# Optimization experiments

Measured on AMD Instinct MI355X. Metric: run time of the kernel, lower is better.

The kernel has to match this reference:

```python
import jax, jax.numpy as jnp
import numpy as np

NUM_HEADS = 12
NUM_LANDMARKS = 64
DIM = 768


def _iterative_inv(mat, n_iter=6):
    # mat: [B, H, L, L]
    L = mat.shape[-1]
    I = jnp.eye(L, dtype=mat.dtype)
    K = mat
    # init: V = K^T / max_j(sum_i K_ij), scalar per (B, H)
    denom = jnp.max(jnp.sum(K, axis=-2), axis=-1)[:, :, None, None]
    V = (1.0 / denom) * jnp.swapaxes(K, -1, -2)
    for _ in range(n_iter):
        KV = jnp.matmul(K, V)
        V = jnp.matmul(0.25 * V, 13.0 * I - jnp.matmul(KV, 15.0 * I - jnp.matmul(KV, 7.0 * I - KV)))
    return V


def setup_inputs() -> dict:
    key = jax.random.key(0)
    k1, k2, k3, k4 = jax.random.split(key, 4)
    B, N, C = 4, 4096, DIM
    x = jax.random.normal(k1, (B, N, C), dtype=jnp.float32)
    w_qkv = jax.random.normal(k2, (3 * C, C), dtype=jnp.float32) * (C ** -0.5)
    w_proj = jax.random.normal(k3, (C, C), dtype=jnp.float32) * (C ** -0.5)
    b_proj = jax.random.normal(k4, (C,), dtype=jnp.float32) * 0.01
    return {"x": x, "w_qkv": w_qkv, "w_proj": w_proj, "b_proj": b_proj}


def reference(x, w_qkv, w_proj, b_proj):
    B, N, C = x.shape
    H, Lm = NUM_HEADS, NUM_LANDMARKS
    hd = C // H
    scale = hd ** 0.5
    # qkv: [3, B, H, N, hd]
    qkv = (x @ w_qkv.T).reshape(B, N, 3, H, hd).transpose(2, 0, 3, 1, 4)
    q, k, v = qkv[0], qkv[1], qkv[2]
    q = q / scale  # scaling happens BEFORE landmark pooling, as in source
    segs = N // Lm  # N % Lm == 0 path
    keys_landmarks = k.reshape(B, H, Lm, segs, hd).mean(axis=-2)      # [B,H,Lm,hd]
    queries_landmarks = q.reshape(B, H, Lm, segs, hd).mean(axis=-2)   # [B,H,Lm,hd]
    kernel_1 = jax.nn.softmax(jnp.einsum('bhnd,bhld->bhnl', q, keys_landmarks), axis=-1)            # [B,H,N,Lm]
    kernel_2 = jax.nn.softmax(jnp.einsum('bhmd,bhld->bhml', queries_landmarks, keys_landmarks), axis=-1)  # [B,H,Lm,Lm]
    kernel_3 = jax.nn.softmax(jnp.einsum('bhld,bhnd->bhln', queries_landmarks, k), axis=-1)         # [B,H,Lm,N]
    out = jnp.matmul(jnp.matmul(kernel_1, _iterative_inv(kernel_2)), jnp.matmul(kernel_3, v))       # [B,H,N,hd]
    out = out.transpose(0, 2, 1, 3).reshape(B, N, C)
    return out @ w_proj.T + b_proj
```

## Files before the change

### kernel.cpp

```cpp
#include <hip/hip_runtime.h>
#include <hip/hip_bf16.h>

#define DI __device__ __forceinline__

typedef __attribute__((ext_vector_type(8))) short bh8;
typedef __attribute__((ext_vector_type(8))) unsigned short us8;
typedef __attribute__((ext_vector_type(4))) float f4ev;

static constexpr int Bn = 4;
static constexpr int Nn = 4096;
static constexpr int Cn = 768;
static constexpr int Hn = 12;
static constexpr int Dn = 64;
static constexpr int Ln = 64;
static constexpr int TOKS = Bn * Nn;
static constexpr int BHn = Bn * Hn;

static constexpr size_t SZ_XB  = (size_t)TOKS * Cn * 2;
static constexpr size_t SZ_QKV = (size_t)BHn * Nn * Dn * 2;
static constexpr size_t OFF_XB   = 0;
static constexpr size_t OFF_QB   = OFF_XB + SZ_XB;
static constexpr size_t OFF_KB   = OFF_QB + SZ_QKV;
static constexpr size_t OFF_VB   = OFF_KB + SZ_QKV;
static constexpr size_t OFF_WQB  = OFF_VB + SZ_QKV;
static constexpr size_t OFF_WPB  = OFF_WQB + (size_t)3 * Cn * Cn * 2;
static constexpr size_t OFF_XM   = OFF_WPB + (size_t)Cn * Cn * 2;
static constexpr size_t OFF_QL   = OFF_XM + (size_t)Bn * Ln * Cn * 4;
static constexpr size_t OFF_KL   = OFF_QL + (size_t)Bn * Ln * Cn * 4;
static constexpr size_t OFF_VINV = OFF_KL + (size_t)Bn * Ln * Cn * 4;
static constexpr size_t OFF_CP   = OFF_VINV + (size_t)BHn * 64 * 64 * 4;
static constexpr size_t OFF_W2   = OFF_CP + (size_t)BHn * 32 * 64 * 2 * 4;

DI unsigned short f2bf(float f) {
  __hip_bfloat16 h = __float2bfloat16(f);
  return *reinterpret_cast<unsigned short*>(&h);
}
DI float bf2f(unsigned short u) {
  union { unsigned int i; float f; } c; c.i = ((unsigned)u) << 16; return c.f;
}

DI void gload_lds16(const void* g, void* l) {
  __builtin_amdgcn_global_load_lds((const __attribute__((address_space(1))) void*)g,
                                   (__attribute__((address_space(3))) void*)l, 16, 0, 0);
}

__global__ void cast_k(const float* __restrict__ s, unsigned short* __restrict__ d, int n4) {
  int i = blockIdx.x * blockDim.x + threadIdx.x;
  int st = gridDim.x * blockDim.x;
  const float4* s4 = (const float4*)s;
  ushort4* d4 = (ushort4*)d;
  for (; i < n4; i += st) {
    float4 v = s4[i];
    ushort4 o; o.x = f2bf(v.x); o.y = f2bf(v.y); o.z = f2bf(v.z); o.w = f2bf(v.w);
    d4[i] = o;
  }
}

__global__ void castmean_k(const float* __restrict__ x, unsigned short* __restrict__ xb,
                           float* __restrict__ xm) {
  int bl = blockIdx.x, cz = blockIdx.y;
  int c = cz * 384 + threadIdx.x * 2;
  const float* xp = x + (size_t)bl * 64 * Cn + c;
  unsigned short* xbp = xb + (size_t)bl * 64 * Cn + c;
  float s0 = 0.f, s1 = 0.f;
  #pragma unroll 8
  for (int r = 0; r < 64; ++r) {
    float2 v = *(const float2*)(xp + (size_t)r * Cn);
    ushort2 o; o.x = f2bf(v.x); o.y = f2bf(v.y);
    *(ushort2*)(xbp + (size_t)r * Cn) = o;
    s0 += v.x; s1 += v.y;
  }
  xm[(size_t)bl * Cn + c]     = s0 * 0.015625f;
  xm[(size_t)bl * Cn + c + 1] = s1 * 0.015625f;
}

__launch_bounds__(256)
__global__ void landgemm_k(const float* __restrict__ xm, const float* __restrict__ wqkv,
                           float* __restrict__ part) {
  __shared__ float XT[64][65];
  __shared__ float WT[64][65];
  int b = blockIdx.x, ct = blockIdx.y, kc = blockIdx.z;
  int t = threadIdx.x;
  int tr = t >> 4, tc = t & 15;
  int r0 = tr * 4, j0 = tc * 4;
  const float* xb_ = xm + (size_t)b * Ln * Cn + kc * 64;
  const float* wb_ = wqkv + (size_t)ct * 64 * Cn + kc * 64;
  #pragma unroll
  for (int i = t; i < 1024; i += 256) {
    int r = i >> 4, c4 = (i & 15) * 4;
    float4 xv = *(const float4*)(xb_ + (size_t)r * Cn + c4);
    XT[c4 + 0][r] = xv.x; XT[c4 + 1][r] = xv.y; XT[c4 + 2][r] = xv.z; XT[c4 + 3][r] = xv.w;
    float4 wv = *(const float4*)(wb_ + (size_t)r * Cn + c4);
    WT[c4 + 0][r] = wv.x; WT[c4 + 1][r] = wv.y; WT[c4 + 2][r] = wv.z; WT[c4 + 3][r] = wv.w;
  }
  __syncthreads();
  float acc[4][4];
  #pragma unroll
  for (int i = 0; i < 4; ++i)
    #pragma unroll
    for (int j = 0; j < 4; ++j) acc[i][j] = 0.f;
  for (int cc = 0; cc < 64; ++cc) {
    float4 a4 = *(const float4*)&XT[cc][r0];
    float4 b4 = *(const float4*)&WT[cc][j0];
    acc[0][0] += a4.x * b4.x; acc[0][1] += a4.x * b4.y; acc[0][2] += a4.x * b4.z; acc[0][3] += a4.x * b4.w;
    acc[1][0] += a4.y * b4.x; acc[1][1] += a4.y * b4.y; acc[1][2] += a4.y * b4.z; acc[1][3] += a4.y * b4.w;
    acc[2][0] += a4.z * b4.x; acc[2][1] += a4.z * b4.y; acc[2][2] += a4.z * b4.z; acc[2][3] += a4.z * b4.w;
    acc[3][0] += a4.w * b4.x; acc[3][1] += a4.w * b4.y; acc[3][2] += a4.w * b4.z; acc[3][3] += a4.w * b4.w;
  }
  float* op = part + ((size_t)kc * 256 + b * Ln) * 1536 + (size_t)ct * 64;
  #pragma unroll
  for (int i = 0; i < 4; ++i)
    *(float4*)(op + (size_t)(r0 + i) * 1536 + j0) = make_float4(acc[i][0], acc[i][1], acc[i][2], acc[i][3]);
}

__global__ void landred_k(const float* __restrict__ part, float* __restrict__ ql,
                          float* __restrict__ kl) {
  int i4 = blockIdx.x * 256 + threadIdx.x;
  const float4* p4 = (const float4*)part;
  float4 s = p4[i4];
  #pragma unroll
  for (int kc = 1; kc < 12; ++kc) {
    float4 v = p4[(size_t)kc * 98304 + i4];
    s.x += v.x; s.y += v.y; s.z += v.z; s.w += v.w;
  }
  int row = i4 / 384, c = (i4 % 384) * 4;
  if (c < 768) {
    s.x *= 0.125f; s.y *= 0.125f; s.z *= 0.125f; s.w *= 0.125f;
    *(float4*)(ql + (size_t)row * Cn + c) = s;
  } else {
    *(float4*)(kl + (size_t)row * Cn + (c - 768)) = s;
  }
}

__launch_bounds__(256)
__global__ void k2inv_k(const float* __restrict__ ql, const float* __restrict__ kl,
                        float* __restrict__ vinv) {
  __shared__ float B0[64][68], B1[64][68], B2[64][68], B3[64][68],
                   B4[64][68], B5[64][68], B6[64][68], B7[64][68];
  __shared__ float dinv_s;
  float (*Qt)[68] = B0, (*Kt)[68] = B1;
  float (*KV)[68] = B0, (*KVt)[68] = B1;
  float (*K2)[68] = B2, (*K2t)[68] = B3;
  float (*Vv)[68] = B4, (*Vt)[68] = B5;
  float (*T1)[68] = B6, (*Uu)[68] = B7;

  int bh = blockIdx.x, b = bh / Hn, h = bh % Hn;
  int t = threadIdx.x;
  int tr = t >> 4, tc = t & 15;
  int r0 = tr * 4, j0 = tc * 4;

  {
    const float* qbase = ql + (size_t)(b * Ln) * Cn + h * Dn;
    const float* kbase = kl + (size_t)(b * Ln) * Cn + h * Dn;
    #pragma unroll
    for (int it = 0; it < 4; ++it) {
      int idx = it * 256 + t;
      int l = idx >> 4, d0 = (idx & 15) * 4;
      float4 qv = *(const float4*)(qbase + (size_t)l * Cn + d0);
      float4 kv = *(const float4*)(kbase + (size_t)l * Cn + d0);
      Qt[d0 + 0][l] = qv.x; Qt[d0 + 1][l] = qv.y; Qt[d0 + 2][l] = qv.z; Qt[d0 + 3][l] = qv.w;
      Kt[d0 + 0][l] = kv.x; Kt[d0 + 1][l] = kv.y; Kt[d0 + 2][l] = kv.z; Kt[d0 + 3][l] = kv.w;
    }
  }
  __syncthreads();

  float acc[4][4];
  #define MM64(LT, RR)                                                     \
    {                                                                      \
      _Pragma("unroll")                                                    \
      for (int i_ = 0; i_ < 4; ++i_)                                       \
        _Pragma("unroll")                                                  \
        for (int j_ = 0; j_ < 4; ++j_) acc[i_][j_] = 0.f;                  \
      for (int c_ = 0; c_ < 64; c_ += 4) {                                 \
        _Pragma("unroll")                                                  \
        for (int cc_ = 0; cc_ < 4; ++cc_) {                                \
          float4 a4 = *(const float4*)&LT[c_ + cc_][r0];                   \
          float4 b4 = *(const float4*)&RR[c_ + cc_][j0];                   \
          acc[0][0] += a4.x * b4.x; acc[0][1] += a4.x * b4.y;              \
          acc[0][2] += a4.x * b4.z; acc[0][3] += a4.x * b4.w;              \
          acc[1][0] += a4.y * b4.x; acc[1][1] += a4.y * b4.y;              \
          acc[1][2] += a4.y * b4.z; acc[1][3] += a4.y * b4.w;              \
          acc[2][0] += a4.z * b4.x; acc[2][1] += a4.z * b4.y;              \
          acc[2][2] += a4.z * b4.z; acc[2][3] += a4.z * b4.w;              \
          acc[3][0] += a4.w * b4.x; acc[3][1] += a4.w * b4.y;              \
          acc[3][2] += a4.w * b4.z; acc[3][3] += a4.w * b4.w;              \
        }                                                                  \
      }                                                                    \
    }

  MM64(Qt, Kt);
  #pragma unroll
  for (int i = 0; i < 4; ++i)
    *(float4*)&K2[r0 + i][j0] = make_float4(acc[i][0], acc[i][1], acc[i][2], acc[i][3]);
  __syncthreads();

  if (t < 64) {
    float m = -1e30f;
    #pragma unroll
    for (int c4 = 0; c4 < 16; ++c4) {
      float4 v = *(const float4*)&K2[t][c4 * 4];
      m = fmaxf(m, fmaxf(fmaxf(v.x, v.y), fmaxf(v.z, v.w)));
    }
    float s = 0.f;
    #pragma unroll
    for (int c4 = 0; c4 < 16; ++c4) {
      float4 v = *(const float4*)&K2[t][c4 * 4];
      v.x = __expf(v.x - m); v.y = __expf(v.y - m);
      v.z = __expf(v.z - m); v.w = __expf(v.w - m);
      s += v.x + v.y + v.z + v.w;
      *(float4*)&K2[t][c4 * 4] = v;
    }
    float inv = 1.f / s;
    #pragma unroll
    for (int c4 = 0; c4 < 16; ++c4) {
      float4 v = *(const float4*)&K2[t][c4 * 4];
      v.x *= inv; v.y *= inv; v.z *= inv; v.w *= inv;
      *(float4*)&K2[t][c4 * 4] = v;
      K2t[c4 * 4 + 0][t] = v.x; K2t[c4 * 4 + 1][t] = v.y;
      K2t[c4 * 4 + 2][t] = v.z; K2t[c4 * 4 + 3][t] = v.w;
    }
  }
  __syncthreads();
  if (t < 64) {
    float cs = 0.f;
    #pragma unroll
    for (int c4 = 0; c4 < 16; ++c4) {
      float4 v = *(const float4*)&K2t[t][c4 * 4];
      cs += v.x + v.y + v.z + v.w;
    }
    #pragma unroll
    for (int off = 1; off < 64; off <<= 1) cs = fmaxf(cs, __shfl_xor(cs, off));
    if (t == 0) dinv_s = 1.f / cs;
  }
  __syncthreads();
  float dinv = dinv_s;
  #pragma unroll
  for (int jj = 0; jj < 4; ++jj) {
    float4 k4 = *(const float4*)&K2[j0 + jj][r0];
    k4.x *= dinv; k4.y *= dinv; k4.z *= dinv; k4.w *= dinv;
    *(float4*)&Vt[j0 + jj][r0] = k4;
    Vv[r0 + 0][j0 + jj] = k4.x; Vv[r0 + 1][j0 + jj] = k4.y;
    Vv[r0 + 2][j0 + jj] = k4.z; Vv[r0 + 3][j0 + jj] = k4.w;
  }
  __syncthreads();

  float nv[4][4];
  for (int itn = 0; itn < 6; ++itn) {
    MM64(K2t, Vv);
    #pragma unroll
    for (int i = 0; i < 4; ++i)
      *(float4*)&KV[r0 + i][j0] = make_float4(acc[i][0], acc[i][1], acc[i][2], acc[i][3]);
    #pragma unroll
    for (int jj = 0; jj < 4; ++jj)
      *(float4*)&KVt[j0 + jj][r0] = make_float4(acc[0][jj], acc[1][jj], acc[2][jj], acc[3][jj]);
    __syncthreads();
    MM64(KVt, KV);
    #pragma unroll
    for (int i = 0; i < 4; ++i) {
      float4 kv4 = *(const float4*)&KV[r0 + i][j0];
      *(float4*)&T1[r0 + i][j0] = make_float4(7.f * kv4.x - acc[i][0], 7.f * kv4.y - acc[i][1],
                                              7.f * kv4.z - acc[i][2], 7.f * kv4.w - acc[i][3]);
    }
    __syncthreads();
    MM64(KVt, T1);
    #pragma unroll
    for (int i = 0; i < 4; ++i) {
      float4 kv4 = *(const float4*)&KV[r0 + i][j0];
      *(float4*)&Uu[r0 + i][j0] = make_float4(15.f * kv4.x - acc[i][0], 15.f * kv4.y - acc[i][1],
                                              15.f * kv4.z - acc[i][2], 15.f * kv4.w - acc[i][3]);
    }
    __syncthreads();
    MM64(Vt, Uu);
    #pragma unroll
    for (int i = 0; i < 4; ++i) {
      float4 v4 = *(const float4*)&Vv[r0 + i][j0];
      nv[i][0] = 0.25f * (13.f * v4.x - acc[i][0]);
      nv[i][1] = 0.25f * (13.f * v4.y - acc[i][1]);
      nv[i][2] = 0.25f * (13.f * v4.z - acc[i][2]);
      nv[i][3] = 0.25f * (13.f * v4.w - acc[i][3]);
    }
    __syncthreads();
    #pragma unroll
    for (int i = 0; i < 4; ++i)
      *(float4*)&Vv[r0 + i][j0] = make_float4(nv[i][0], nv[i][1], nv[i][2], nv[i][3]);
    #pragma unroll
    for (int jj = 0; jj < 4; ++jj)
      *(float4*)&Vt[j0 + jj][r0] = make_float4(nv[0][jj], nv[1][jj], nv[2][jj], nv[3][jj]);
    __syncthreads();
  }
  float* op = vinv + (size_t)bh * 4096;
  #pragma unroll
  for (int i = 0; i < 4; ++i)
    *(float4*)(op + (size_t)(r0 + i) * 64 + j0) = make_float4(nv[i][0], nv[i][1], nv[i][2], nv[i][3]);
  #undef MM64
}

__launch_bounds__(256)
__global__ void gemm_qkv_k(const __hip_bfloat16* __restrict__ A, const __hip_bfloat16* __restrict__ W,
                           __hip_bfloat16* __restrict__ qb, __hip_bfloat16* __restrict__ kb,
                           __hip_bfloat16* __restrict__ vb) {
  __shared__ unsigned short As[2][128][64], Bs[2][128][64];
  int t = threadIdx.x, lane = t & 63, w = t >> 6;
  int wr = w >> 1, wc = w & 1;
  int m0 = blockIdx.x * 128, n0 = blockIdx.y * 128;
  int srow = w * 8 + (lane >> 3);
  int scol = ((lane & 7) ^ ((lane >> 3) & 7)) * 8;
  f4ev acc[4][4];
  f4ev zz = {0.f, 0.f, 0.f, 0.f};
  #pragma unroll
  for (int m = 0; m < 4; ++m)
    #pragma unroll
    for (int n = 0; n < 4; ++n) acc[m][n] = zz;
  const __hip_bfloat16* ga = A + (size_t)(m0 + srow) * Cn + scol;
  const __hip_bfloat16* gb = W + (size_t)(n0 + srow) * Cn + scol;

  #pragma unroll
  for (int c = 0; c < 4; ++c) {
    gload_lds16(ga + (size_t)(c * 32) * Cn, &As[0][c * 32 + w * 8][0]);
    gload_lds16(gb + (size_t)(c * 32) * Cn, &Bs[0][c * 32 + w * 8][0]);
  }
  __syncthreads();
  int cur = 0;
  for (int it = 0; it < 12; ++it) {
    if (it < 11) {
      int k0 = (it + 1) * 64;
      #pragma unroll
      for (int c = 0; c < 4; ++c) {
        gload_lds16(ga + (size_t)(c * 32) * Cn + k0, &As[cur ^ 1][c * 32 + w * 8][0]);
        gload_lds16(gb + (size_t)(c * 32) * Cn + k0, &Bs[cur ^ 1][c * 32 + w * 8][0]);
      }
    }
    #pragma unroll
    for (int ks = 0; ks < 2; ++ks) {
      int pc = ((ks * 4 + (lane >> 4)) ^ (lane & 7)) * 8;
      bh8 af[4], bf_[4];
      #pragma unroll
      for (int m = 0; m < 4; ++m)
        af[m] = *(const bh8*)&As[cur][wr * 64 + m * 16 + (lane & 15)][pc];
      #pragma unroll
      for (int n = 0; n < 4; ++n)
        bf_[n] = *(const bh8*)&Bs[cur][wc * 64 + n * 16 + (lane & 15)][pc];
      #pragma unroll
      for (int m = 0; m < 4; ++m)
        #pragma unroll
        for (int n = 0; n < 4; ++n)
          acc[m][n] = __builtin_amdgcn_mfma_f32_16x16x32_bf16(af[m], bf_[n], acc[m][n], 0, 0, 0);
    }
    __syncthreads();
    cur ^= 1;
  }
  int which = (n0 >= 1536) ? 2 : (n0 >= 768 ? 1 : 0);
  __hip_bfloat16* dst = which == 0 ? qb : (which == 1 ? kb : vb);
  float sc = which == 0 ? 0.125f : 1.f;
  #pragma unroll
  for (int m = 0; m < 4; ++m) {
    int rbase = m0 + wr * 64 + m * 16 + ((lane >> 4) << 2);
    #pragma unroll
    for (int n = 0; n < 4; ++n) {
      int c = n0 + wc * 64 + n * 16 + (lane & 15);
      int rem = c - which * 768;
      int h = rem >> 6, dd = rem & 63;
      #pragma unroll
      for (int jj = 0; jj < 4; ++jj) {
        int r = rbase + jj;
        int b = r >> 12, ntok = r & 4095;
        dst[(((size_t)(b * Hn + h) * Nn + ntok) << 6) + dd] = __float2bfloat16(acc[m][n][jj] * sc);
      }
    }
  }
}

__launch_bounds__(256)
__global__ void k3vflash_k(const float* __restrict__ ql, const __hip_bfloat16* __restrict__ kb,
                           const __hip_bfloat16* __restrict__ vb,
                           float* __restrict__ ocp, float* __restrict__ stat) {
  __shared__ unsigned short Ks[128][72];
  __shared__ unsigned short VT[64][136];
  auto Pl = (unsigned short (*)[136]) & Ks[0][0];
  int ch = blockIdx.x, bh = blockIdx.y;
  int b = bh / Hn, h = bh % Hn;
  int t = threadIdx.x, lane = t & 63, w = t >> 6;

  {
    int row = t >> 1, half = (t & 1) * 32;
    const us8* krow = (const us8*)((const unsigned short*)kb + ((size_t)bh * Nn + (size_t)ch * 128 + row) * Dn + half);
    const us8* vrow = (const us8*)((const unsigned short*)vb + ((size_t)bh * Nn + (size_t)ch * 128 + row) * Dn + half);
    us8 kv0 = krow[0], kv1 = krow[1], kv2 = krow[2], kv3 = krow[3];
    us8 vv0 = vrow[0], vv1 = vrow[1], vv2 = vrow[2], vv3 = vrow[3];
    *(us8*)&Ks[row][half + 0]  = kv0;
    *(us8*)&Ks[row][half + 8]  = kv1;
    *(us8*)&Ks[row][half + 16] = kv2;
    *(us8*)&Ks[row][half + 24] = kv3;
    #pragma unroll
    for (int e = 0; e < 8; ++e) {
      VT[half + e][row]      = vv0[e];
      VT[half + 8 + e][row]  = vv1[e];
      VT[half + 16 + e][row] = vv2[e];
      VT[half + 24 + e][row] = vv3[e];
    }
  }
  bh8 aq[2];
  {
    const float* qrow = ql + ((size_t)(b * Ln + w * 16 + (lane & 15))) * Cn + h * Dn + (lane >> 4) * 8;
    #pragma unroll
    for (int ks = 0; ks < 2; ++ks) {
      float4 f0 = *(const float4*)(qrow + ks * 32);
      float4 f1 = *(const float4*)(qrow + ks * 32 + 4);
      bh8 v;
      v[0] = (short)f2bf(f0.x); v[1] = (short)f2bf(f0.y); v[2] = (short)f2bf(f0.z); v[3] = (short)f2bf(f0.w);
      v[4] = (short)f2bf(f1.x); v[5] = (short)f2bf(f1.y); v[6] = (short)f2bf(f1.z); v[7] = (short)f2bf(f1.w);
      aq[ks] = v;
    }
  }
  __syncthreads();
  f4ev sacc[8];
  f4ev zz = {0.f, 0.f, 0.f, 0.f};
  #pragma unroll
  for (int nt = 0; nt < 8; ++nt) sacc[nt] = zz;
  #pragma unroll
  for (int ks = 0; ks < 2; ++ks)
    #pragma unroll
    for (int nt = 0; nt < 8; ++nt) {
      bh8 bk = *(const bh8*)&Ks[nt * 16 + (lane & 15)][ks * 32 + (lane >> 4) * 8];
      sacc[nt] = __builtin_amdgcn_mfma_f32_16x16x32_bf16(aq[ks], bk, sacc[nt], 0, 0, 0);
    }
  float M[4];
  #pragma unroll
  for (int j = 0; j < 4; ++j) {
    float m = sacc[0][j];
    #pragma unroll
    for (int nt = 1; nt < 8; ++nt) m = fmaxf(m, sacc[nt][j]);
    m = fmaxf(m, __shfl_xor(m, 1));
    m = fmaxf(m, __shfl_xor(m, 2));
    m = fmaxf(m, __shfl_xor(m, 4));
    m = fmaxf(m, __shfl_xor(m, 8));
    M[j] = m;
  }
  __syncthreads();
  float Ssum[4] = {0.f, 0.f, 0.f, 0.f};
  #pragma unroll
  for (int nt = 0; nt < 8; ++nt)
    #pragma unroll
    for (int j = 0; j < 4; ++j) {
      float pf = __expf(sacc[nt][j] - M[j]);
      Ssum[j] += pf;
      Pl[w * 16 + (lane >> 4) * 4 + j][nt * 16 + (lane & 15)] = f2bf(pf);
    }
  #pragma unroll
  for (int j = 0; j < 4; ++j) {
    float s = Ssum[j];
    s += __shfl_xor(s, 1);
    s += __shfl_xor(s, 2);
    s += __shfl_xor(s, 4);
    s += __shfl_xor(s, 8);
    Ssum[j] = s;
  }
  if ((lane & 15) == 0) {
    #pragma unroll
    for (int j = 0; j < 4; ++j) {
      int l2 = w * 16 + (lane >> 4) * 4 + j;
      float* sp = stat + (((size_t)bh * 32 + ch) * 64 + l2) * 2;
      sp[0] = M[j]; sp[1] = Ssum[j];
    }
  }
  __syncthreads();
  f4ev oacc[4];
  #pragma unroll
  for (int nt = 0; nt < 4; ++nt) oacc[nt] = zz;
  #pragma unroll
  for (int ks = 0; ks < 4; ++ks) {
    bh8 ap = *(const bh8*)&Pl[w * 16 + (lane & 15)][ks * 32 + (lane >> 4) * 8];
    #pragma unroll
    for (int nt = 0; nt < 4; ++nt) {
      bh8 bv = *(const bh8*)&VT[nt * 16 + (lane & 15)][ks * 32 + (lane >> 4) * 8];
      oacc[nt] = __builtin_amdgcn_mfma_f32_16x16x32_bf16(ap, bv, oacc[nt], 0, 0, 0);
    }
  }
  float* ob = ocp + (((size_t)bh * 32 + ch) * 64) * 64;
  #pragma unroll
  for (int nt = 0; nt < 4; ++nt)
    #pragma unroll
    for (int j = 0; j < 4; ++j) {
      int l2 = w * 16 + ((lane >> 4) << 2) + j;
      ob[l2 * 64 + nt * 16 + (lane & 15)] = oacc[nt][j];
    }
}

__global__ void w2f_k(const float* __restrict__ ocp, const float* __restrict__ stat,
                      const float* __restrict__ vinv, float* __restrict__ w2) {
  __shared__ float kv[64][72], vi[64][72];
  __shared__ float wch[32][64];
  __shared__ float invS[64];
  int bh = blockIdx.x, t = threadIdx.x, j = t & 63, ig = t >> 6;
  if (t < 64) {
    const float* sp = stat + (size_t)bh * 32 * 128;
    float M = -1e30f;
    #pragma unroll
    for (int c = 0; c < 32; ++c) M = fmaxf(M, sp[c * 128 + t * 2]);
    float S = 0.f;
    #pragma unroll
    for (int c = 0; c < 32; ++c) {
      float wcb = __expf(sp[c * 128 + t * 2] - M);
      wch[c][t] = wcb;
      S += wcb * sp[c * 128 + t * 2 + 1];
    }
    invS[t] = 1.f / S;
  }
  for (int i = t; i < 4096; i += 256) vi[i >> 6][i & 63] = vinv[(size_t)bh * 4096 + i];
  __syncthreads();
  float acc[16];
  #pragma unroll
  for (int i = 0; i < 16; ++i) acc[i] = 0.f;
  const float* op = ocp + (size_t)bh * 32 * 4096;
  for (int c = 0; c < 32; ++c) {
    #pragma unroll
    for (int jj = 0; jj < 4; ++jj) {
      int i4 = t * 4 + jj * 1024;
      float4 v = *(const float4*)(op + (size_t)c * 4096 + i4);
      float wcb = wch[c][i4 >> 6];
      acc[jj * 4 + 0] += v.x * wcb;
      acc[jj * 4 + 1] += v.y * wcb;
      acc[jj * 4 + 2] += v.z * wcb;
      acc[jj * 4 + 3] += v.w * wcb;
    }
  }
  #pragma unroll
  for (int jj = 0; jj < 4; ++jj) {
    int i4 = t * 4 + jj * 1024;
    float is = invS[i4 >> 6];
    kv[i4 >> 6][(i4 & 63) + 0] = acc[jj * 4 + 0] * is;
    kv[i4 >> 6][(i4 & 63) + 1] = acc[jj * 4 + 1] * is;
    kv[i4 >> 6][(i4 & 63) + 2] = acc[jj * 4 + 2] * is;
    kv[i4 >> 6][(i4 & 63) + 3] = acc[jj * 4 + 3] * is;
  }
  __syncthreads();
  float a[16];
  #pragma unroll
  for (int li = 0; li < 16; ++li) a[li] = 0.f;
  for (int c2 = 0; c2 < 64; ++c2) {
    float vv = kv[c2][j];
    #pragma unroll
    for (int li = 0; li < 16; ++li) a[li] += vi[ig * 16 + li][c2] * vv;
  }
  #pragma unroll
  for (int li = 0; li < 16; ++li) w2[(size_t)bh * 4096 + (ig * 16 + li) * 64 + j] = a[li];
}

__launch_bounds__(256)
__global__ void k1app_k(const __hip_bfloat16* __restrict__ qb, const float* __restrict__ kl,
                        const float* __restrict__ w2, __hip_bfloat16* __restrict__ oh) {
  __shared__ unsigned short SM[128 * 72 + 64 * 72 * 2];
  auto Klhi = (unsigned short (*)[72])(SM);
  auto Kllo = (unsigned short (*)[72])(SM + 64 * 72);
  auto Pl   = (unsigned short (*)[72])(SM);
  auto Whi  = (unsigned short (*)[72])(SM + 128 * 72);
  auto Wlo  = (unsigned short (*)[72])(SM + 128 * 72 + 64 * 72);

  int ch = blockIdx.x, bh = blockIdx.y;
  int b = bh / Hn, h = bh % Hn;
  int t = threadIdx.x, lane = t & 63, w = t >> 6;

  {
    const float* klb = kl + (size_t)(b * Ln) * Cn + h * Dn;
    const float* w2b = w2 + (size_t)bh * 4096;
    #pragma unroll
    for (int it = 0; it < 4; ++it) {
      int idx = it * 256 + t;
      int l = idx >> 4, d0 = (idx & 15) * 4;
      float4 kv = *(const float4*)(klb + (size_t)l * Cn + d0);
      ushort4 hi4; ushort4 lo4;
      hi4.x = f2bf(kv.x); lo4.x = f2bf(kv.x - bf2f(hi4.x));
      hi4.y = f2bf(kv.y); lo4.y = f2bf(kv.y - bf2f(hi4.y));
      hi4.z = f2bf(kv.z); lo4.z = f2bf(kv.z - bf2f(hi4.z));
      hi4.w = f2bf(kv.w); lo4.w = f2bf(kv.w - bf2f(hi4.w));
      *(ushort4*)&Klhi[l][d0] = hi4;
      *(ushort4*)&Kllo[l][d0] = lo4;
      float4 wv = *(const float4*)(w2b + (size_t)l * 64 + d0);
      unsigned short h0 = f2bf(wv.x), h1 = f2bf(wv.y), h2 = f2bf(wv.z), h3 = f2bf(wv.w);
      Whi[d0 + 0][l] = h0; Wlo[d0 + 0][l] = f2bf(wv.x - bf2f(h0));
      Whi[d0 + 1][l] = h1; Wlo[d0 + 1][l] = f2bf(wv.y - bf2f(h1));
      Whi[d0 + 2][l] = h2; Wlo[d0 + 2][l] = f2bf(wv.z - bf2f(h2));
      Whi[d0 + 3][l] = h3; Wlo[d0 + 3][l] = f2bf(wv.w - bf2f(h3));
    }
  }
  bh8 aq[2][2];
  {
    const unsigned short* qbase = (const unsigned short*)qb + ((size_t)bh * Nn + (size_t)ch * 128) * Dn;
    #pragma unroll
    for (int m = 0; m < 2; ++m)
      #pragma unroll
      for (int ks = 0; ks < 2; ++ks)
        aq[m][ks] = *(const bh8*)(qbase + (size_t)(w * 32 + m * 16 + (lane & 15)) * Dn + ks * 32 + (lane >> 4) * 8);
  }
  __syncthreads();
  f4ev sacc[2][4];
  f4ev zz = {0.f, 0.f, 0.f, 0.f};
  #pragma unroll
  for (int m = 0; m < 2; ++m)
    #pragma unroll
    for (int nt = 0; nt < 4; ++nt) sacc[m][nt] = zz;
  #pragma unroll
  for (int ks = 0; ks < 2; ++ks)
    #pragma unroll
    for (int nt = 0; nt < 4; ++nt) {
      bh8 bhi = *(const bh8*)&Klhi[nt * 16 + (lane & 15)][ks * 32 + (lane >> 4) * 8];
      bh8 blo = *(const bh8*)&Kllo[nt * 16 + (lane & 15)][ks * 32 + (lane >> 4) * 8];
      #pragma unroll
      for (int m = 0; m < 2; ++m) {
        sacc[m][nt] = __builtin_amdgcn_mfma_f32_16x16x32_bf16(aq[m][ks], bhi, sacc[m][nt], 0, 0, 0);
        sacc[m][nt] = __builtin_amdgcn_mfma_f32_16x16x32_bf16(aq[m][ks], blo, sacc[m][nt], 0, 0, 0);
      }
    }
  float Pn[2][4][4];
  #pragma unroll
  for (int m = 0; m < 2; ++m)
    #pragma unroll
    for (int j = 0; j < 4; ++j) {
      float mx = sacc[m][0][j];
      #pragma unroll
      for (int nt = 1; nt < 4; ++nt) mx = fmaxf(mx, sacc[m][nt][j]);
      mx = fmaxf(mx, __shfl_xor(mx, 1));
      mx = fmaxf(mx, __shfl_xor(mx, 2));
      mx = fmaxf(mx, __shfl_xor(mx, 4));
      mx = fmaxf(mx, __shfl_xor(mx, 8));
      float sum = 0.f;
      #pragma unroll
      for (int nt = 0; nt < 4; ++nt) {
        float e = __expf(sacc[m][nt][j] - mx);
        Pn[m][nt][j] = e;
        sum += e;
      }
      sum += __shfl_xor(sum, 1);
      sum += __shfl_xor(sum, 2);
      sum += __shfl_xor(sum, 4);
      sum += __shfl_xor(sum, 8);
      float inv = 1.f / sum;
      #pragma unroll
      for (int nt = 0; nt < 4; ++nt) Pn[m][nt][j] *= inv;
    }
  __syncthreads();
  #pragma unroll
  for (int m = 0; m < 2; ++m)
    #pragma unroll
    for (int nt = 0; nt < 4; ++nt)
      #pragma unroll
      for (int j = 0; j < 4; ++j)
        Pl[w * 32 + m * 16 + (lane >> 4) * 4 + j][nt * 16 + (lane & 15)] = f2bf(Pn[m][nt][j]);
  __syncthreads();
  f4ev oacc[2][4];
  #pragma unroll
  for (int m = 0; m < 2; ++m)
    #pragma unroll
    for (int nt = 0; nt < 4; ++nt) oacc[m][nt] = zz;
  #pragma unroll
  for (int ks = 0; ks < 2; ++ks) {
    bh8 ap[2];
    #pragma unroll
    for (int m = 0; m < 2; ++m)
      ap[m] = *(const bh8*)&Pl[w * 32 + m * 16 + (lane & 15)][ks * 32 + (lane >> 4) * 8];
    #pragma unroll
    for (int nt = 0; nt < 4; ++nt) {
      bh8 bhi = *(const bh8*)&Whi[nt * 16 + (lane & 15)][ks * 32 + (lane >> 4) * 8];
      bh8 blo = *(const bh8*)&Wlo[nt * 16 + (lane & 15)][ks * 32 + (lane >> 4) * 8];
      #pragma unroll
      for (int m = 0; m < 2; ++m) {
        oacc[m][nt] = __builtin_amdgcn_mfma_f32_16x16x32_bf16(ap[m], bhi, oacc[m][nt], 0, 0, 0);
        oacc[m][nt] = __builtin_amdgcn_mfma_f32_16x16x32_bf16(ap[m], blo, oacc[m][nt], 0, 0, 0);
      }
    }
  }
  unsigned short* ohb = (unsigned short*)oh;
  #pragma unroll
  for (int m = 0; m < 2; ++m)
    #pragma unroll
    for (int nt = 0; nt < 4; ++nt)
      #pragma unroll
      for (int j = 0; j < 4; ++j) {
        int tok = ch * 128 + w * 32 + m * 16 + (lane >> 4) * 4 + j;
        int dd = nt * 16 + (lane & 15);
        ohb[((size_t)(b * Nn + tok)) * Cn + h * Dn + dd] = f2bf(oacc[m][nt][j]);
      }
}

__launch_bounds__(256)
__global__ void gemm_proj_k(const __hip_bfloat16* __restrict__ A, const __hip_bfloat16* __restrict__ W,
                            const float* __restrict__ bias, float* __restrict__ out) {
  __shared__ unsigned short As[128][32], Bs[128][32];
  int orig = blockIdx.x;
  int wg = (orig & 7) * 96 + (orig >> 3);
  int mt = wg / 6, ntile = wg % 6;
  int m0 = mt * 128, n0 = ntile * 128;
  int t = threadIdx.x, lane = t & 63, w = t >> 6;
  int wr = w >> 1, wc = w & 1;
  int srow = lane >> 2;
  int scol = (((lane & 3) ^ ((lane >> 3) & 3))) * 8;
  int rcol = (((lane >> 4) ^ ((lane >> 1) & 3))) * 8;
  f4ev acc[4][4];
  f4ev zz = {0.f, 0.f, 0.f, 0.f};
  #pragma unroll
  for (int m = 0; m < 4; ++m)
    #pragma unroll
    for (int n = 0; n < 4; ++n) acc[m][n] = zz;
  const __hip_bfloat16* ga = A + (size_t)(m0 + w * 16 + srow) * Cn + scol;
  const __hip_bfloat16* gb = W + (size_t)(n0 + w * 16 + srow) * Cn + scol;
  for (int k0 = 0; k0 < Cn; k0 += 32) {
    gload_lds16(ga + k0,                   &As[w * 16][0]);
    gload_lds16(ga + (size_t)64 * Cn + k0, &As[64 + w * 16][0]);
    gload_lds16(gb + k0,                   &Bs[w * 16][0]);
    gload_lds16(gb + (size_t)64 * Cn + k0, &Bs[64 + w * 16][0]);
    __syncthreads();
    bh8 af[4], bf_[4];
    #pragma unroll
    for (int m = 0; m < 4; ++m)
      af[m] = *(const bh8*)&As[wr * 64 + m * 16 + (lane & 15)][rcol];
    #pragma unroll
    for (int n = 0; n < 4; ++n)
      bf_[n] = *(const bh8*)&Bs[wc * 64 + n * 16 + (lane & 15)][rcol];
    #pragma unroll
    for (int m = 0; m < 4; ++m)
      #pragma unroll
      for (int n = 0; n < 4; ++n)
        acc[m][n] = __builtin_amdgcn_mfma_f32_16x16x32_bf16(af[m], bf_[n], acc[m][n], 0, 0, 0);
    __syncthreads();
  }
  #pragma unroll
  for (int m = 0; m < 4; ++m) {
    int rbase = m0 + wr * 64 + m * 16 + ((lane >> 4) << 2);
    #pragma unroll
    for (int n = 0; n < 4; ++n) {
      int c = n0 + wc * 64 + n * 16 + (lane & 15);
      float bv = bias[c];
      #pragma unroll
      for (int jj = 0; jj < 4; ++jj)
        out[(size_t)(rbase + jj) * Cn + c] = acc[m][n][jj] + bv;
    }
  }
}

extern "C" void kernel_launch(void* const* d_in, const int* in_sizes, int n_in,
                              void* d_out, int out_size, void* d_ws, size_t ws_size,
                              hipStream_t stream) {
  const float* x     = (const float*)d_in[0];
  const float* wqkv  = (const float*)d_in[1];
  const float* wproj = (const float*)d_in[2];
  const float* bproj = (const float*)d_in[3];
  float* out = (float*)d_out;
  char* ws = (char*)d_ws;

  auto xb   = (__hip_bfloat16*)(ws + OFF_XB);
  auto qb   = (__hip_bfloat16*)(ws + OFF_QB);
  auto kb   = (__hip_bfloat16*)(ws + OFF_KB);
  auto vb   = (__hip_bfloat16*)(ws + OFF_VB);
  auto wqb  = (__hip_bfloat16*)(ws + OFF_WQB);
  auto wpb  = (__hip_bfloat16*)(ws + OFF_WPB);
  auto ocp  = (float*)(ws + OFF_XB);
  auto oh   = (__hip_bfloat16*)(ws + OFF_XB);
  auto part = (float*)(ws + OFF_QB);
  auto xm   = (float*)(ws + OFF_XM);
  auto ql   = (float*)(ws + OFF_QL);
  auto kl   = (float*)(ws + OFF_KL);
  auto vinv = (float*)(ws + OFF_VINV);
  auto cp   = (float*)(ws + OFF_CP);
  auto w2   = (float*)(ws + OFF_W2);

  castmean_k<<<dim3(256, 2), 192, 0, stream>>>(x, (unsigned short*)xb, xm);
  cast_k<<<1024, 256, 0, stream>>>(wqkv, (unsigned short*)wqb, 3 * Cn * Cn / 4);
  cast_k<<<512, 256, 0, stream>>>(wproj, (unsigned short*)wpb, Cn * Cn / 4);
  landgemm_k<<<dim3(4, 24, 12), 256, 0, stream>>>(xm, wqkv, part);
  landred_k<<<384, 256, 0, stream>>>(part, ql, kl);
  k2inv_k<<<48, 256, 0, stream>>>(ql, kl, vinv);
  gemm_qkv_k<<<dim3(128, 18), 256, 0, stream>>>(xb, wqb, qb, kb, vb);
  k3vflash_k<<<dim3(32, 48), 256, 0, stream>>>(ql, kb, vb, ocp, cp);
  w2f_k<<<48, 256, 0, stream>>>(ocp, cp, vinv, w2);
  k1app_k<<<dim3(32, 48), 256, 0, stream>>>(qb, kl, w2, oh);
  gemm_proj_k<<<768, 256, 0, stream>>>(oh, wpb, bproj, out);
}
```

Measured before the change: 257.9 us.

## Loop k3vflash over four key chunks with online softmax; reorder GEMM grid rasterization

The k3vflash kernel now processes 512 keys per block in four 128-key stages, carrying a running max and sum (online softmax). This cuts its grid from 32 to 8 chunks per head and shrinks the partial outputs and stats that w2f_k must reduce. The QKV and projection GEMM grids are also swapped so that N tiles vary fastest, and the custom swizzle in gemm_proj is dropped, which changes L2 reuse of the A rows. The trade-offs are fewer blocks (384) for k3vflash, extra barriers per stage, and possibly worse cache locality in gemm_proj without the swizzle.

```diff
diff --git a/kernel.cpp b/kernel.cpp
--- a/kernel.cpp
+++ b/kernel.cpp
@@ -302,7 +302,7 @@
   __shared__ unsigned short As[2][128][64], Bs[2][128][64];
   int t = threadIdx.x, lane = t & 63, w = t >> 6;
   int wr = w >> 1, wc = w & 1;
-  int m0 = blockIdx.x * 128, n0 = blockIdx.y * 128;
+  int n0 = blockIdx.x * 128, m0 = blockIdx.y * 128;
   int srow = w * 8 + (lane >> 3);
   int scol = ((lane & 7) ^ ((lane >> 3) & 7)) * 8;
   f4ev acc[4][4];
@@ -381,24 +381,6 @@
   int b = bh / Hn, h = bh % Hn;
   int t = threadIdx.x, lane = t & 63, w = t >> 6;
 
-  {
-    int row = t >> 1, half = (t & 1) * 32;
-    const us8* krow = (const us8*)((const unsigned short*)kb + ((size_t)bh * Nn + (size_t)ch * 128 + row) * Dn + half);
-    const us8* vrow = (const us8*)((const unsigned short*)vb + ((size_t)bh * Nn + (size_t)ch * 128 + row) * Dn + half);
-    us8 kv0 = krow[0], kv1 = krow[1], kv2 = krow[2], kv3 = krow[3];
-    us8 vv0 = vrow[0], vv1 = vrow[1], vv2 = vrow[2], vv3 = vrow[3];
-    *(us8*)&Ks[row][half + 0]  = kv0;
-    *(us8*)&Ks[row][half + 8]  = kv1;
-    *(us8*)&Ks[row][half + 16] = kv2;
-    *(us8*)&Ks[row][half + 24] = kv3;
-    #pragma unroll
-    for (int e = 0; e < 8; ++e) {
-      VT[half + e][row]      = vv0[e];
-      VT[half + 8 + e][row]  = vv1[e];
-      VT[half + 16 + e][row] = vv2[e];
-      VT[half + 24 + e][row] = vv3[e];
-    }
-  }
   bh8 aq[2];
   {
     const float* qrow = ql + ((size_t)(b * Ln + w * 16 + (lane & 15))) * Cn + h * Dn + (lane >> 4) * 8;
@@ -412,71 +394,104 @@
       aq[ks] = v;
     }
   }
-  __syncthreads();
-  f4ev sacc[8];
+  float Mrun[4], Srun[4];
+  #pragma unroll
+  for (int j = 0; j < 4; ++j) { Mrun[j] = -1e30f; Srun[j] = 0.f; }
+  f4ev oacc[4];
   f4ev zz = {0.f, 0.f, 0.f, 0.f};
   #pragma unroll
-  for (int nt = 0; nt < 8; ++nt) sacc[nt] = zz;
-  #pragma unroll
-  for (int ks = 0; ks < 2; ++ks)
-    #pragma unroll
-    for (int nt = 0; nt < 8; ++nt) {
-      bh8 bk = *(const bh8*)&Ks[nt * 16 + (lane & 15)][ks * 32 + (lane >> 4) * 8];
-      sacc[nt] = __builtin_amdgcn_mfma_f32_16x16x32_bf16(aq[ks], bk, sacc[nt], 0, 0, 0);
-    }
-  float M[4];
-  #pragma unroll
-  for (int j = 0; j < 4; ++j) {
-    float m = sacc[0][j];
-    #pragma unroll
-    for (int nt = 1; nt < 8; ++nt) m = fmaxf(m, sacc[nt][j]);
-    m = fmaxf(m, __shfl_xor(m, 1));
-    m = fmaxf(m, __shfl_xor(m, 2));
-    m = fmaxf(m, __shfl_xor(m, 4));
-    m = fmaxf(m, __shfl_xor(m, 8));
-    M[j] = m;
-  }
-  __syncthreads();
-  float Ssum[4] = {0.f, 0.f, 0.f, 0.f};
-  #pragma unroll
-  for (int nt = 0; nt < 8; ++nt)
+  for (int nt = 0; nt < 4; ++nt) oacc[nt] = zz;
+
+  const unsigned short* kbase0 = (const unsigned short*)kb + ((size_t)bh * Nn + (size_t)ch * 512) * Dn;
+  const unsigned short* vbase0 = (const unsigned short*)vb + ((size_t)bh * Nn + (size_t)ch * 512) * Dn;
+
+  for (int st4 = 0; st4 < 4; ++st4) {
+    __syncthreads();
+    {
+      int row = t >> 1, half = (t & 1) * 32;
+      const us8* krow = (const us8*)(kbase0 + (size_t)(st4 * 128 + row) * Dn + half);
+      const us8* vrow = (const us8*)(vbase0 + (size_t)(st4 * 128 + row) * Dn + half);
+      us8 kv0 = krow[0], kv1 = krow[1], kv2 = krow[2], kv3 = krow[3];
+      us8 vv0 = vrow[0], vv1 = vrow[1], vv2 = vrow[2], vv3 = vrow[3];
+      *(us8*)&Ks[row][half + 0]  = kv0;
+      *(us8*)&Ks[row][half + 8]  = kv1;
+      *(us8*)&Ks[row][half + 16] = kv2;
+      *(us8*)&Ks[row][half + 24] = kv3;
+      #pragma unroll
+      for (int e = 0; e < 8; ++e) {
+        VT[half + e][row]      = vv0[e];
+        VT[half + 8 + e][row]  = vv1[e];
+        VT[half + 16 + e][row] = vv2[e];
+        VT[half + 24 + e][row] = vv3[e];
+      }
+    }
+    __syncthreads();
+    f4ev sacc[8];
+    #pragma unroll
+    for (int nt = 0; nt < 8; ++nt) sacc[nt] = zz;
+    #pragma unroll
+    for (int ks = 0; ks < 2; ++ks)
+      #pragma unroll
+      for (int nt = 0; nt < 8; ++nt) {
+        bh8 bk = *(const bh8*)&Ks[nt * 16 + (lane & 15)][ks * 32 + (lane >> 4) * 8];
+        sacc[nt] = __builtin_amdgcn_mfma_f32_16x16x32_bf16(aq[ks], bk, sacc[nt], 0, 0, 0);
+      }
+    float scale[4];
     #pragma unroll
     for (int j = 0; j < 4; ++j) {
-      float pf = __expf(sacc[nt][j] - M[j]);
-      Ssum[j] += pf;
-      Pl[w * 16 + (lane >> 4) * 4 + j][nt * 16 + (lane & 15)] = f2bf(pf);
-    }
-  #pragma unroll
-  for (int j = 0; j < 4; ++j) {
-    float s = Ssum[j];
-    s += __shfl_xor(s, 1);
-    s += __shfl_xor(s, 2);
-    s += __shfl_xor(s, 4);
-    s += __shfl_xor(s, 8);
-    Ssum[j] = s;
+      float m = sacc[0][j];
+      #pragma unroll
+      for (int nt = 1; nt < 8; ++nt) m = fmaxf(m, sacc[nt][j]);
+      m = fmaxf(m, __shfl_xor(m, 1));
+      m = fmaxf(m, __shfl_xor(m, 2));
+      m = fmaxf(m, __shfl_xor(m, 4));
+      m = fmaxf(m, __shfl_xor(m, 8));
+      float mn = fmaxf(Mrun[j], m);
+      scale[j] = __expf(Mrun[j] - mn);
+      Mrun[j] = mn;
+    }
+    __syncthreads();
+    float Sadd[4] = {0.f, 0.f, 0.f, 0.f};
+    #pragma unroll
+    for (int nt = 0; nt < 8; ++nt)
+      #pragma unroll
+      for (int j = 0; j < 4; ++j) {
+        float pf = __expf(sacc[nt][j] - Mrun[j]);
+        Sadd[j] += pf;
+        Pl[w * 16 + (lane >> 4) * 4 + j][nt * 16 + (lane & 15)] = f2bf(pf);
+      }
+    #pragma unroll
+    for (int j = 0; j < 4; ++j) {
+      float s = Sadd[j];
+      s += __shfl_xor(s, 1);
+      s += __shfl_xor(s, 2);
+      s += __shfl_xor(s, 4);
+      s += __shfl_xor(s, 8);
+      Srun[j] = Srun[j] * scale[j] + s;
+    }
+    #pragma unroll
+    for (int nt = 0; nt < 4; ++nt)
+      #pragma unroll
+      for (int j = 0; j < 4; ++j) oacc[nt][j] *= scale[j];
+    #pragma unroll
+    for (int ks = 0; ks < 4; ++ks) {
+      bh8 ap = *(const bh8*)&Pl[w * 16 + (lane & 15)][ks * 32 + (lane >> 4) * 8];
+      #pragma unroll
+      for (int nt = 0; nt < 4; ++nt) {
+        bh8 bv = *(const bh8*)&VT[nt * 16 + (lane & 15)][ks * 32 + (lane >> 4) * 8];
+        oacc[nt] = __builtin_amdgcn_mfma_f32_16x16x32_bf16(ap, bv, oacc[nt], 0, 0, 0);
+      }
+    }
   }
   if ((lane & 15) == 0) {
     #pragma unroll
     for (int j = 0; j < 4; ++j) {
       int l2 = w * 16 + (lane >> 4) * 4 + j;
-      float* sp = stat + (((size_t)bh * 32 + ch) * 64 + l2) * 2;
-      sp[0] = M[j]; sp[1] = Ssum[j];
-    }
-  }
-  __syncthreads();
-  f4ev oacc[4];
-  #pragma unroll
-  for (int nt = 0; nt < 4; ++nt) oacc[nt] = zz;
-  #pragma unroll
-  for (int ks = 0; ks < 4; ++ks) {
-    bh8 ap = *(const bh8*)&Pl[w * 16 + (lane & 15)][ks * 32 + (lane >> 4) * 8];
-    #pragma unroll
-    for (int nt = 0; nt < 4; ++nt) {
-      bh8 bv = *(const bh8*)&VT[nt * 16 + (lane & 15)][ks * 32 + (lane >> 4) * 8];
-      oacc[nt] = __builtin_amdgcn_mfma_f32_16x16x32_bf16(ap, bv, oacc[nt], 0, 0, 0);
-    }
-  }
-  float* ob = ocp + (((size_t)bh * 32 + ch) * 64) * 64;
+      float* sp = stat + (((size_t)bh * 8 + ch) * 64 + l2) * 2;
+      sp[0] = Mrun[j]; sp[1] = Srun[j];
+    }
+  }
+  float* ob = ocp + ((size_t)bh * 8 + ch) * 4096;
   #pragma unroll
   for (int nt = 0; nt < 4; ++nt)
     #pragma unroll
@@ -489,17 +504,17 @@
 __global__ void w2f_k(const float* __restrict__ ocp, const float* __restrict__ stat,
                       const float* __restrict__ vinv, float* __restrict__ w2) {
   __shared__ float kv[64][72], vi[64][72];
-  __shared__ float wch[32][64];
+  __shared__ float wch[8][64];
   __shared__ float invS[64];
   int bh = blockIdx.x, t = threadIdx.x, j = t & 63, ig = t >> 6;
   if (t < 64) {
-    const float* sp = stat + (size_t)bh * 32 * 128;
+    const float* sp = stat + (size_t)bh * 8 * 128;
     float M = -1e30f;
     #pragma unroll
-    for (int c = 0; c < 32; ++c) M = fmaxf(M, sp[c * 128 + t * 2]);
+    for (int c = 0; c < 8; ++c) M = fmaxf(M, sp[c * 128 + t * 2]);
     float S = 0.f;
     #pragma unroll
-    for (int c = 0; c < 32; ++c) {
+    for (int c = 0; c < 8; ++c) {
       float wcb = __expf(sp[c * 128 + t * 2] - M);
       wch[c][t] = wcb;
       S += wcb * sp[c * 128 + t * 2 + 1];
@@ -511,8 +526,8 @@
   float acc[16];
   #pragma unroll
   for (int i = 0; i < 16; ++i) acc[i] = 0.f;
-  const float* op = ocp + (size_t)bh * 32 * 4096;
-  for (int c = 0; c < 32; ++c) {
+  const float* op = ocp + (size_t)bh * 8 * 4096;
+  for (int c = 0; c < 8; ++c) {
     #pragma unroll
     for (int jj = 0; jj < 4; ++jj) {
       int i4 = t * 4 + jj * 1024;
@@ -686,10 +701,7 @@
 __global__ void gemm_proj_k(const __hip_bfloat16* __restrict__ A, const __hip_bfloat16* __restrict__ W,
                             const float* __restrict__ bias, float* __restrict__ out) {
   __shared__ unsigned short As[128][32], Bs[128][32];
-  int orig = blockIdx.x;
-  int wg = (orig & 7) * 96 + (orig >> 3);
-  int mt = wg / 6, ntile = wg % 6;
-  int m0 = mt * 128, n0 = ntile * 128;
+  int n0 = blockIdx.x * 128, m0 = blockIdx.y * 128;
   int t = threadIdx.x, lane = t & 63, w = t >> 6;
   int wr = w >> 1, wc = w & 1;
   int srow = lane >> 2;
@@ -769,9 +781,9 @@
   landgemm_k<<<dim3(4, 24, 12), 256, 0, stream>>>(xm, wqkv, part);
   landred_k<<<384, 256, 0, stream>>>(part, ql, kl);
   k2inv_k<<<48, 256, 0, stream>>>(ql, kl, vinv);
-  gemm_qkv_k<<<dim3(128, 18), 256, 0, stream>>>(xb, wqb, qb, kb, vb);
-  k3vflash_k<<<dim3(32, 48), 256, 0, stream>>>(ql, kb, vb, ocp, cp);
+  gemm_qkv_k<<<dim3(18, 128), 256, 0, stream>>>(xb, wqb, qb, kb, vb);
+  k3vflash_k<<<dim3(8, 48), 256, 0, stream>>>(ql, kb, vb, ocp, cp);
   w2f_k<<<48, 256, 0, stream>>>(ocp, cp, vinv, w2);
   k1app_k<<<dim3(32, 48), 256, 0, stream>>>(qb, kl, w2, oh);
-  gemm_proj_k<<<768, 256, 0, stream>>>(oh, wpb, bproj, out);
-}
+  gemm_proj_k<<<dim3(6, 128), 256, 0, stream>>>(oh, wpb, bproj, out);
+}
```

Measured after the change: 264.5 us. +2.5%, slower.
